# Performance work log

Measured on AMD Instinct MI355X. Metric: run time of the kernel, lower is better.

Reference implementation:

```python
import jax, jax.numpy as jnp
import numpy as np

FILTERS = 256
KH, KW = 3, 3
SH, SW = 1, 1
IN_CH = 128


def setup_inputs() -> dict:
    key = jax.random.key(0)
    k1, k2 = jax.random.split(key)
    inputs = jax.random.normal(k1, (32, 112, 112, IN_CH), dtype=jnp.float32)
    # Glorot-uniform init matching the layer's build()
    limit = np.sqrt(6.0 / (KH * KW * IN_CH + FILTERS)).astype(np.float32)
    kernel = jax.random.uniform(k2, (KH, KW, IN_CH, FILTERS), dtype=jnp.float32,
                                minval=-limit, maxval=limit)
    bias = jnp.zeros((FILTERS,), dtype=jnp.float32)
    return {"inputs": inputs, "kernel": kernel, "bias": bias}


def reference(inputs, kernel, bias):
    # Equivalent math to extract_patches(SAME) + flattened matmul + bias:
    # a standard 2D convolution in NHWC with HWIO kernel.
    out = jax.lax.conv_general_dilated(
        inputs, kernel,
        window_strides=(SH, SW),
        padding="SAME",
        dimension_numbers=("NHWC", "HWIO", "NHWC"),
    )
    return out + bias
```

## Files before the change

### kernel.cpp

```cpp
#include <hip/hip_runtime.h>

typedef __attribute__((ext_vector_type(4)))  float   floatx4;
typedef __attribute__((ext_vector_type(16))) float   floatx16;
typedef __attribute__((ext_vector_type(8)))  __bf16  bf16x8;
typedef unsigned short ushort_t;
typedef __attribute__((ext_vector_type(8)))  ushort_t ushortx8;

typedef const unsigned int __attribute__((address_space(1)))* gptr_t;
typedef unsigned int __attribute__((address_space(3)))* lptr_t;

#define NIMG 32
#define H    112
#define W    112
#define CIN  128
#define COUT 256
#define HP   114
#define WP   114
#define HW   12544

#define BM 256
#define BN 256
#define BK 64
#define NT 18

#define PREPAD_BLOCKS 12996
#define WTRANS_BLOCKS 1152

__device__ __forceinline__ ushort_t f32_to_bf16(float f) {
    unsigned u = __float_as_uint(f);
    unsigned r = 0x7fffu + ((u >> 16) & 1u);
    return (ushort_t)((u + r) >> 16);
}

__global__ __launch_bounds__(256) void prepass_fused(const float* __restrict__ in,
                                                     const float* __restrict__ k,
                                                     ushort_t* __restrict__ pad,
                                                     ushort_t* __restrict__ wt) {
    int bid = blockIdx.x;
    if (bid < PREPAD_BLOCKS) {
        int u    = bid * 256 + threadIdx.x;
        int ic16 = u & 7;
        int sp   = u >> 3;
        int iw   = sp % WP;
        int sp2  = sp / WP;
        int ih   = sp2 % HP;
        int n    = sp2 / HP;
        ushortx8 v0, v1;
        if (ih >= 1 && ih <= H && iw >= 1 && iw <= W) {
            const float* src = in + ((size_t)((n * H + (ih - 1)) * W + (iw - 1))) * CIN + ic16 * 16;
            floatx4 a = *reinterpret_cast<const floatx4*>(src);
            floatx4 b = *reinterpret_cast<const floatx4*>(src + 4);
            floatx4 c = *reinterpret_cast<const floatx4*>(src + 8);
            floatx4 d = *reinterpret_cast<const floatx4*>(src + 12);
#pragma unroll
            for (int j = 0; j < 4; ++j) {
                v0[j] = f32_to_bf16(a[j]); v0[4 + j] = f32_to_bf16(b[j]);
                v1[j] = f32_to_bf16(c[j]); v1[4 + j] = f32_to_bf16(d[j]);
            }
        } else {
#pragma unroll
            for (int j = 0; j < 8; ++j) { v0[j] = 0; v1[j] = 0; }
        }
        ushortx8* dst = reinterpret_cast<ushortx8*>(pad) + ((size_t)sp * 16 + ic16 * 2);
        dst[0] = v0;
        dst[1] = v1;
    } else {
        int t    = (bid - PREPAD_BLOCKS) * 256 + threadIdx.x;
        int ic   = t & 127;
        int oc   = (t >> 7) & 255;
        int khkw = t >> 15;
        wt[t] = f32_to_bf16(k[((size_t)(khkw * CIN + ic)) * COUT + oc]);
    }
}

__device__ __forceinline__ int aoffK(int t) {
    int tap = t >> 1;
    return ((tap / 3) * WP + (tap % 3)) * CIN + (t & 1) * 64;
}
__device__ __forceinline__ int boffK(int t) {
    int tap = t >> 1;
    return tap * (COUT * CIN) + (t & 1) * 64;
}


__global__ __launch_bounds__(512, 2) void conv_mfma8(const ushort_t* __restrict__ pad,
                                                     const ushort_t* __restrict__ wt,
                                                     const float* __restrict__ bias,
                                                     float* __restrict__ out) {
    __shared__ __align__(16) ushort_t lds[32768];

    const int tid  = threadIdx.x;
    const int wid  = tid >> 6;
    const int lane = tid & 63;
    const int wm   = wid >> 2;
    const int wn   = wid & 3;
    const int bid  = blockIdx.x;
    const int bm   = (bid & 7) * 196 + (bid >> 3);

    const int rb   = (tid & 255) >> 3;
    const int half = tid >> 8;
    const int lc   = (tid & 7) ^ (rb & 7) ^ ((rb >> 3) & 3);

    const ushort_t* srcAc[4];
#pragma unroll
    for (int q = 0; q < 4; ++q) {
        int m  = bm * BM + half * 128 + q * 32 + rb;
        int n  = m / HW;
        int r  = m % HW;
        int oh = r / W;
        int ow = r % W;
        srcAc[q] = pad + ((size_t)((n * HP + oh) * WP + ow)) * CIN + lc * 8;
    }
    const ushort_t* srcB[4];
#pragma unroll
    for (int i = 0; i < 4; ++i)
        srcB[i] = wt + (size_t)(i * 64 + ((tid >> 3) & 63)) * CIN
                     + ((((tid & 7) ^ ((tid >> 3) & 7) ^ ((tid >> 6) & 3))) * 8);

    const int awBase   = (wid >> 2) * 8192 + (wid & 3) * 512;
    const int dstSlotB = wid * 512;

#define STAGE_AC(q_, oA)                                                                            \
    __builtin_amdgcn_global_load_lds((gptr_t)(srcAc[q_] + (oA)),                                    \
                                     (lptr_t)&lds[(q_) * 2048 + awBase], 16, 0, 0);
#define STAGE_B1(j_, oB)                                                                            \
    __builtin_amdgcn_global_load_lds((gptr_t)(srcB[j_] + (oB)),                                     \
                                     (lptr_t)&lds[16384 + (j_) * 4096 + dstSlotB], 16, 0, 0);

    const int aBase = (wm * 128 + (lane & 31)) * 64;
    const int bBase = 16384 + (wn * 64 + (lane & 31)) * 64;
    const int gr    = (lane & 7) ^ ((lane >> 3) & 3);
    int cOff[4];
#pragma unroll
    for (int ksl = 0; ksl < 4; ++ksl)
        cOff[ksl] = ((ksl * 2 + (lane >> 5)) ^ gr) * 8;

    floatx16 acc[4][2];
#pragma unroll
    for (int i = 0; i < 4; ++i)
#pragma unroll
        for (int j = 0; j < 2; ++j) acc[i][j] = (floatx16)0.0f;

    {
        const int oA0 = aoffK(0);
        const int oB0 = boffK(0);
        STAGE_AC(0, oA0); STAGE_AC(1, oA0); STAGE_AC(2, oA0);
        STAGE_B1(0, oB0); STAGE_B1(1, oB0); STAGE_B1(2, oB0); STAGE_B1(3, oB0);
    }
    asm volatile("s_waitcnt vmcnt(0)" ::: "memory");
    __builtin_amdgcn_s_barrier();

    for (int t = 0; t < NT; ++t) {
        const int oAc = aoffK(t);
        const int oAn = aoffK(t + 1);
        const int oBn = boffK(t + 1);
        bf16x8 bfr[2][4];
#pragma unroll
        for (int q = 0; q < 4; ++q) {
            bf16x8 af[4];
#pragma unroll
            for (int ksl = 0; ksl < 4; ++ksl)
                af[ksl] = *reinterpret_cast<const bf16x8*>(&lds[aBase + q * 2048 + cOff[ksl]]);
            if (q == 0) {
#pragma unroll
                for (int ksl = 0; ksl < 4; ++ksl)
                    bfr[0][ksl] = *reinterpret_cast<const bf16x8*>(&lds[bBase + cOff[ksl]]);
            }
            if (q == 0) { STAGE_AC(3, oAc); }
            if (q == 1 && t + 1 < NT) { STAGE_AC(0, oAn); STAGE_B1(0, oBn); STAGE_B1(1, oBn); }
            if (q == 2 && t + 1 < NT) { STAGE_AC(1, oAn); STAGE_B1(2, oBn); STAGE_B1(3, oBn); }
            if (q == 3 && t + 1 < NT) { STAGE_AC(2, oAn); }
            __builtin_amdgcn_s_barrier();
            __builtin_amdgcn_s_setprio(1);
            if (q == 0) {
#pragma unroll
                for (int ksl = 0; ksl < 4; ++ksl)
                    acc[0][0] = __builtin_amdgcn_mfma_f32_32x32x16_bf16(af[ksl], bfr[0][ksl], acc[0][0], 0, 0, 0);
#pragma unroll
                for (int ksl = 0; ksl < 4; ++ksl)
                    bfr[1][ksl] = *reinterpret_cast<const bf16x8*>(&lds[bBase + 2048 + cOff[ksl]]);
#pragma unroll
                for (int ksl = 0; ksl < 4; ++ksl)
                    acc[0][1] = __builtin_amdgcn_mfma_f32_32x32x16_bf16(af[ksl], bfr[1][ksl], acc[0][1], 0, 0, 0);
            } else {
#pragma unroll
                for (int ksl = 0; ksl < 4; ++ksl) {
                    acc[q][0] = __builtin_amdgcn_mfma_f32_32x32x16_bf16(af[ksl], bfr[0][ksl], acc[q][0], 0, 0, 0);
                    acc[q][1] = __builtin_amdgcn_mfma_f32_32x32x16_bf16(af[ksl], bfr[1][ksl], acc[q][1], 0, 0, 0);
                }
            }
            __builtin_amdgcn_s_setprio(0);
            if (q == 1) {
                if (t < NT - 1) { asm volatile("s_waitcnt vmcnt(4)" ::: "memory"); }
                else            { asm volatile("s_waitcnt vmcnt(1)" ::: "memory"); }
            }
            if (q == 2) {
                if (t < NT - 1) { asm volatile("s_waitcnt vmcnt(6)" ::: "memory"); }
                else            { asm volatile("s_waitcnt vmcnt(0)" ::: "memory"); }
            }
            if (q == 3) { asm volatile("s_waitcnt vmcnt(1)" ::: "memory"); }
            __builtin_amdgcn_s_barrier();
        }
    }

    const int colL = wn * 64 + (lane & 31);
    const int rowL = bm * BM + wm * 128 + 4 * (lane >> 5);
    float bv[2];
#pragma unroll
    for (int cb = 0; cb < 2; ++cb) bv[cb] = bias[colL + cb * 32];
#pragma unroll
    for (int q = 0; q < 4; ++q)
#pragma unroll
        for (int cb = 0; cb < 2; ++cb)
#pragma unroll
            for (int reg = 0; reg < 16; ++reg) {
                int row = rowL + q * 32 + (reg & 3) + 8 * (reg >> 2);
                out[(size_t)row * COUT + colL + cb * 32] = acc[q][cb][reg] + bv[cb];
            }
#undef STAGE_AC
#undef STAGE_B1
}

extern "C" void kernel_launch(void* const* d_in, const int* in_sizes, int n_in,
                              void* d_out, int out_size, void* d_ws, size_t ws_size,
                              hipStream_t stream) {
    const float* input = (const float*)d_in[0];
    const float* kern  = (const float*)d_in[1];
    const float* bias  = (const float*)d_in[2];
    float* out         = (float*)d_out;

    ushort_t* pad = (ushort_t*)d_ws;
    ushort_t* wt  = pad + (size_t)NIMG * HP * WP * CIN;

    prepass_fused<<<PREPAD_BLOCKS + WTRANS_BLOCKS, 256, 0, stream>>>(input, kern, pad, wt);
    conv_mfma8<<<1568, 512, 0, stream>>>(pad, wt, bias, out);
}
```

Before: 362.6 us.

## Shrink conv GEMM tile to 128x128 with double-buffered A and 4-wave blocks

Replaces the 256x256 tile with 8 waves by a 128x128 tile with 4 waves, giving 6272 blocks and allowing three blocks per CU. The A operand is now double-buffered by parity and the load/wait/barrier schedule is rebuilt around two half-steps per K slice. The goal is better occupancy and latency hiding. In exchange, each tile gets less data reuse, so the kernel issues more global/L2 traffic per FLOP.

```diff
diff --git a/kernel.cpp b/kernel.cpp
--- a/kernel.cpp
+++ b/kernel.cpp
@@ -18,10 +18,10 @@
 #define WP   114
 #define HW   12544
 
-#define BM 256
-#define BN 256
-#define BK 64
+#define BM 128
+#define BN 128
 #define NT 18
+#define NBLK 6272
 
 #define PREPAD_BLOCKS 12996
 #define WTRANS_BLOCKS 1152
@@ -83,51 +83,47 @@
 }
 
 
-__global__ __launch_bounds__(512, 2) void conv_mfma8(const ushort_t* __restrict__ pad,
+__global__ __launch_bounds__(256, 3) void conv_mfma4(const ushort_t* __restrict__ pad,
                                                      const ushort_t* __restrict__ wt,
                                                      const float* __restrict__ bias,
                                                      float* __restrict__ out) {
-    __shared__ __align__(16) ushort_t lds[32768];
+    __shared__ __align__(16) ushort_t lds[24576];
 
     const int tid  = threadIdx.x;
     const int wid  = tid >> 6;
     const int lane = tid & 63;
-    const int wm   = wid >> 2;
-    const int wn   = wid & 3;
+    const int wm   = wid >> 1;
+    const int wn   = wid & 1;
     const int bid  = blockIdx.x;
-    const int bm   = (bid & 7) * 196 + (bid >> 3);
-
-    const int rb   = (tid & 255) >> 3;
-    const int half = tid >> 8;
-    const int lc   = (tid & 7) ^ (rb & 7) ^ ((rb >> 3) & 3);
-
-    const ushort_t* srcAc[4];
-#pragma unroll
-    for (int q = 0; q < 4; ++q) {
-        int m  = bm * BM + half * 128 + q * 32 + rb;
+    const int swz  = (bid & 7) * (NBLK / 8) + (bid >> 3);
+    const int mi   = swz >> 1;
+    const int ni   = swz & 1;
+
+    const int trow = tid >> 3;
+    const int lc   = (tid & 7) ^ (trow & 7) ^ ((trow >> 3) & 3);
+
+    const ushort_t* srcA[4];
+    const ushort_t* srcB[4];
+#pragma unroll
+    for (int s = 0; s < 4; ++s) {
+        int m  = mi * BM + s * 32 + trow;
         int n  = m / HW;
         int r  = m % HW;
         int oh = r / W;
         int ow = r % W;
-        srcAc[q] = pad + ((size_t)((n * HP + oh) * WP + ow)) * CIN + lc * 8;
-    }
-    const ushort_t* srcB[4];
-#pragma unroll
-    for (int i = 0; i < 4; ++i)
-        srcB[i] = wt + (size_t)(i * 64 + ((tid >> 3) & 63)) * CIN
-                     + ((((tid & 7) ^ ((tid >> 3) & 7) ^ ((tid >> 6) & 3))) * 8);
-
-    const int awBase   = (wid >> 2) * 8192 + (wid & 3) * 512;
-    const int dstSlotB = wid * 512;
-
-#define STAGE_AC(q_, oA)                                                                            \
-    __builtin_amdgcn_global_load_lds((gptr_t)(srcAc[q_] + (oA)),                                    \
-                                     (lptr_t)&lds[(q_) * 2048 + awBase], 16, 0, 0);
-#define STAGE_B1(j_, oB)                                                                            \
-    __builtin_amdgcn_global_load_lds((gptr_t)(srcB[j_] + (oB)),                                     \
-                                     (lptr_t)&lds[16384 + (j_) * 4096 + dstSlotB], 16, 0, 0);
-
-    const int aBase = (wm * 128 + (lane & 31)) * 64;
+        srcA[s] = pad + ((size_t)((n * HP + oh) * WP + ow)) * CIN + lc * 8;
+        srcB[s] = wt + (size_t)(ni * BN + s * 32 + trow) * CIN + lc * 8;
+    }
+    const int dstSlot = wid * 512;
+
+#define STAGE_A(par, s_, oA)                                                                        \
+    __builtin_amdgcn_global_load_lds((gptr_t)(srcA[s_] + (oA)),                                     \
+                                     (lptr_t)&lds[(par) * 8192 + (s_) * 2048 + dstSlot], 16, 0, 0);
+#define STAGE_B(s_, oB)                                                                             \
+    __builtin_amdgcn_global_load_lds((gptr_t)(srcB[s_] + (oB)),                                     \
+                                     (lptr_t)&lds[16384 + (s_) * 2048 + dstSlot], 16, 0, 0);
+
+    const int aBase = (wm * 64 + (lane & 31)) * 64;
     const int bBase = 16384 + (wn * 64 + (lane & 31)) * 64;
     const int gr    = (lane & 7) ^ ((lane >> 3) & 3);
     int cOff[4];
@@ -135,90 +131,84 @@
     for (int ksl = 0; ksl < 4; ++ksl)
         cOff[ksl] = ((ksl * 2 + (lane >> 5)) ^ gr) * 8;
 
-    floatx16 acc[4][2];
-#pragma unroll
-    for (int i = 0; i < 4; ++i)
+    floatx16 acc[2][2];
+#pragma unroll
+    for (int i = 0; i < 2; ++i)
 #pragma unroll
         for (int j = 0; j < 2; ++j) acc[i][j] = (floatx16)0.0f;
 
     {
         const int oA0 = aoffK(0);
         const int oB0 = boffK(0);
-        STAGE_AC(0, oA0); STAGE_AC(1, oA0); STAGE_AC(2, oA0);
-        STAGE_B1(0, oB0); STAGE_B1(1, oB0); STAGE_B1(2, oB0); STAGE_B1(3, oB0);
+        STAGE_A(0, 0, oA0); STAGE_A(0, 1, oA0); STAGE_A(0, 2, oA0); STAGE_A(0, 3, oA0);
+        STAGE_B(0, oB0); STAGE_B(1, oB0); STAGE_B(2, oB0); STAGE_B(3, oB0);
     }
     asm volatile("s_waitcnt vmcnt(0)" ::: "memory");
     __builtin_amdgcn_s_barrier();
 
     for (int t = 0; t < NT; ++t) {
-        const int oAc = aoffK(t);
-        const int oAn = aoffK(t + 1);
-        const int oBn = boffK(t + 1);
-        bf16x8 bfr[2][4];
-#pragma unroll
-        for (int q = 0; q < 4; ++q) {
-            bf16x8 af[4];
-#pragma unroll
-            for (int ksl = 0; ksl < 4; ++ksl)
-                af[ksl] = *reinterpret_cast<const bf16x8*>(&lds[aBase + q * 2048 + cOff[ksl]]);
-            if (q == 0) {
-#pragma unroll
-                for (int ksl = 0; ksl < 4; ++ksl)
-                    bfr[0][ksl] = *reinterpret_cast<const bf16x8*>(&lds[bBase + cOff[ksl]]);
+        const int par  = t & 1;
+        const int parn = par ^ 1;
+        const int oAn  = aoffK(t + 1);
+        const int oBn  = boffK(t + 1);
+        const int aB   = par * 8192 + aBase;
+        bf16x8 af[4], bfr0[4], bfr1[4];
+
+#pragma unroll
+        for (int ksl = 0; ksl < 4; ++ksl) {
+            af[ksl]   = *reinterpret_cast<const bf16x8*>(&lds[aB + cOff[ksl]]);
+            bfr0[ksl] = *reinterpret_cast<const bf16x8*>(&lds[bBase + cOff[ksl]]);
+        }
+        if (t + 1 < NT) { STAGE_A(parn, 0, oAn); STAGE_A(parn, 2, oAn); }
+        __builtin_amdgcn_s_setprio(1);
+#pragma unroll
+        for (int ksl = 0; ksl < 4; ++ksl)
+            acc[0][0] = __builtin_amdgcn_mfma_f32_32x32x16_bf16(af[ksl], bfr0[ksl], acc[0][0], 0, 0, 0);
+#pragma unroll
+        for (int ksl = 0; ksl < 4; ++ksl)
+            bfr1[ksl] = *reinterpret_cast<const bf16x8*>(&lds[bBase + 2048 + cOff[ksl]]);
+#pragma unroll
+        for (int ksl = 0; ksl < 4; ++ksl)
+            acc[0][1] = __builtin_amdgcn_mfma_f32_32x32x16_bf16(af[ksl], bfr1[ksl], acc[0][1], 0, 0, 0);
+        __builtin_amdgcn_s_setprio(0);
+        if (t + 1 < NT) { asm volatile("s_waitcnt vmcnt(2)" ::: "memory"); }
+        else            { asm volatile("s_waitcnt vmcnt(0)" ::: "memory"); }
+        __builtin_amdgcn_s_barrier();
+
+#pragma unroll
+        for (int ksl = 0; ksl < 4; ++ksl)
+            af[ksl] = *reinterpret_cast<const bf16x8*>(&lds[aB + 2048 + cOff[ksl]]);
+        if (t + 1 < NT) {
+            STAGE_B(0, oBn); STAGE_B(1, oBn); STAGE_B(2, oBn); STAGE_B(3, oBn);
+            STAGE_A(parn, 1, oAn); STAGE_A(parn, 3, oAn);
+        }
+        __builtin_amdgcn_s_setprio(1);
+#pragma unroll
+        for (int ksl = 0; ksl < 4; ++ksl) {
+            acc[1][0] = __builtin_amdgcn_mfma_f32_32x32x16_bf16(af[ksl], bfr0[ksl], acc[1][0], 0, 0, 0);
+            acc[1][1] = __builtin_amdgcn_mfma_f32_32x32x16_bf16(af[ksl], bfr1[ksl], acc[1][1], 0, 0, 0);
+        }
+        __builtin_amdgcn_s_setprio(0);
+        if (t + 1 < NT) { asm volatile("s_waitcnt vmcnt(2)" ::: "memory"); }
+        __builtin_amdgcn_s_barrier();
+    }
+
+    const int colL = ni * BN + wn * 64 + (lane & 31);
+    const int rowL = mi * BM + wm * 64 + 4 * (lane >> 5);
+    float bv[2];
+#pragma unroll
+    for (int cb = 0; cb < 2; ++cb) bv[cb] = bias[colL + cb * 32];
+#pragma unroll
+    for (int rf = 0; rf < 2; ++rf)
+#pragma unroll
+        for (int cb = 0; cb < 2; ++cb)
+#pragma unroll
+            for (int reg = 0; reg < 16; ++reg) {
+                int row = rowL + rf * 32 + (reg & 3) + 8 * (reg >> 2);
+                out[(size_t)row * COUT + colL + cb * 32] = acc[rf][cb][reg] + bv[cb];
             }
-            if (q == 0) { STAGE_AC(3, oAc); }
-            if (q == 1 && t + 1 < NT) { STAGE_AC(0, oAn); STAGE_B1(0, oBn); STAGE_B1(1, oBn); }
-            if (q == 2 && t + 1 < NT) { STAGE_AC(1, oAn); STAGE_B1(2, oBn); STAGE_B1(3, oBn); }
-            if (q == 3 && t + 1 < NT) { STAGE_AC(2, oAn); }
-            __builtin_amdgcn_s_barrier();
-            __builtin_amdgcn_s_setprio(1);
-            if (q == 0) {
-#pragma unroll
-                for (int ksl = 0; ksl < 4; ++ksl)
-                    acc[0][0] = __builtin_amdgcn_mfma_f32_32x32x16_bf16(af[ksl], bfr[0][ksl], acc[0][0], 0, 0, 0);
-#pragma unroll
-                for (int ksl = 0; ksl < 4; ++ksl)
-                    bfr[1][ksl] = *reinterpret_cast<const bf16x8*>(&lds[bBase + 2048 + cOff[ksl]]);
-#pragma unroll
-                for (int ksl = 0; ksl < 4; ++ksl)
-                    acc[0][1] = __builtin_amdgcn_mfma_f32_32x32x16_bf16(af[ksl], bfr[1][ksl], acc[0][1], 0, 0, 0);
-            } else {
-#pragma unroll
-                for (int ksl = 0; ksl < 4; ++ksl) {
-                    acc[q][0] = __builtin_amdgcn_mfma_f32_32x32x16_bf16(af[ksl], bfr[0][ksl], acc[q][0], 0, 0, 0);
-                    acc[q][1] = __builtin_amdgcn_mfma_f32_32x32x16_bf16(af[ksl], bfr[1][ksl], acc[q][1], 0, 0, 0);
-                }
-            }
-            __builtin_amdgcn_s_setprio(0);
-            if (q == 1) {
-                if (t < NT - 1) { asm volatile("s_waitcnt vmcnt(4)" ::: "memory"); }
-                else            { asm volatile("s_waitcnt vmcnt(1)" ::: "memory"); }
-            }
-            if (q == 2) {
-                if (t < NT - 1) { asm volatile("s_waitcnt vmcnt(6)" ::: "memory"); }
-                else            { asm volatile("s_waitcnt vmcnt(0)" ::: "memory"); }
-            }
-            if (q == 3) { asm volatile("s_waitcnt vmcnt(1)" ::: "memory"); }
-            __builtin_amdgcn_s_barrier();
-        }
-    }
-
-    const int colL = wn * 64 + (lane & 31);
-    const int rowL = bm * BM + wm * 128 + 4 * (lane >> 5);
-    float bv[2];
-#pragma unroll
-    for (int cb = 0; cb < 2; ++cb) bv[cb] = bias[colL + cb * 32];
-#pragma unroll
-    for (int q = 0; q < 4; ++q)
-#pragma unroll
-        for (int cb = 0; cb < 2; ++cb)
-#pragma unroll
-            for (int reg = 0; reg < 16; ++reg) {
-                int row = rowL + q * 32 + (reg & 3) + 8 * (reg >> 2);
-                out[(size_t)row * COUT + colL + cb * 32] = acc[q][cb][reg] + bv[cb];
-            }
-#undef STAGE_AC
-#undef STAGE_B1
+#undef STAGE_A
+#undef STAGE_B
 }
 
 extern "C" void kernel_launch(void* const* d_in, const int* in_sizes, int n_in,
@@ -233,5 +223,5 @@
     ushort_t* wt  = pad + (size_t)NIMG * HP * WP * CIN;
 
     prepass_fused<<<PREPAD_BLOCKS + WTRANS_BLOCKS, 256, 0, stream>>>(input, kern, pad, wt);
-    conv_mfma8<<<1568, 512, 0, stream>>>(pad, wt, bias, out);
-}
+    conv_mfma4<<<NBLK, 256, 0, stream>>>(pad, wt, bias, out);
+}
```

Result: faster. 342.8 us (-5.5%).
